# Optimization experiments

Hardware: AMD Instinct MI355X
Metric: run time of the kernel (lower is better)

## Reference

```python
import jax, jax.numpy as jnp
import numpy as np

IN_F, OUT_F, LAT, B = 1024, 1024, 16, 256


def setup_inputs() -> dict:
    key = jax.random.key(0)
    ks = jax.random.split(key, 6)
    # xavier_normal for weight [in, out]
    std_w = float(np.sqrt(2.0 / (IN_F + OUT_F)))
    weight = jax.random.normal(ks[0], (IN_F, OUT_F), dtype=jnp.float32) * std_w
    bias = jnp.full((OUT_F,), 0.01, dtype=jnp.float32)
    # nn.Linear(latent, in): weight [in, latent], bias [in], kaiming-uniform-ish init
    lim = float(1.0 / np.sqrt(LAT))
    lt_w = jax.random.uniform(ks[1], (IN_F, LAT), minval=-lim, maxval=lim, dtype=jnp.float32)
    lt_b = jax.random.uniform(ks[2], (IN_F,), minval=-lim, maxval=lim, dtype=jnp.float32)
    tensor = jax.random.normal(ks[3], (B, IN_F), dtype=jnp.float32)
    z = jax.random.normal(ks[4], (B, LAT), dtype=jnp.float32)
    return {"tensor": tensor, "z": z, "weight": weight, "bias": bias,
            "lt_w": lt_w, "lt_b": lt_b}


def reference(tensor, z, weight, bias, lt_w, lt_b):
    # s = latent_transform(z): [B, in]
    s = z @ lt_w.T + lt_b
    # Demodulation factor: rsqrt(sum_i (s_i * W_io)^2 + eps) = rsqrt((s^2) @ (W^2) + eps)
    # Algebraically identical to forming the per-sample modulated weight, but
    # never materializes the [B, in, out] tensor.
    factor = jax.lax.rsqrt((s * s) @ (weight * weight) + 1e-8)  # [B, out]
    # x @ (W * s[:, :, None]) == (x * s) @ W
    out = ((tensor * s) @ weight) * factor + bias  # [B, out]
    return out
```

## Files before the change

### kernel.cpp

```cpp
#include <hip/hip_runtime.h>
#include <hip/hip_bf16.h>

constexpr int IN_F  = 1024;
constexpr int OUT_F = 1024;
constexpr int LAT   = 16;
constexpr int BATCH = 256;

typedef __attribute__((ext_vector_type(8))) short  bf16x8;
typedef __attribute__((ext_vector_type(4))) float  f32x4;

static __device__ __forceinline__ unsigned short bf16_bits(float v) {
  __hip_bfloat16 h = __float2bfloat16(v);
  return *reinterpret_cast<unsigned short*>(&h);
}
static __device__ __forceinline__ float bf16_f32(unsigned short u) {
  __hip_bfloat16 h;
  *reinterpret_cast<unsigned short*>(&h) = u;
  return __bfloat162float(h);
}

__global__ __launch_bounds__(512) void fused_mod(
    const float* __restrict__ tensor, const float* __restrict__ z,
    const float* __restrict__ lt_w, const float* __restrict__ lt_b,
    const float* __restrict__ W, const float* __restrict__ bias,
    float* __restrict__ out) {
  __shared__ __attribute__((aligned(16))) __hip_bfloat16 s_lds[32 * 1024];
  __shared__ __attribute__((aligned(16))) __hip_bfloat16 wbuf[8][2][32 * 64];

  const int bid = blockIdx.x;
  const int t = threadIdx.x;
  const int n0 = (bid & 31) * 32;
  const int m0 = (bid >> 5) * 32;
  const int lane = t & 63;
  const int wave = t >> 6;
  const int lm = lane & 15;
  const int h = lane >> 4;

  {
    const int koct = h & 1;
    bf16x8 zfrag[2];
#pragma unroll
    for (int bh = 0; bh < 2; ++bh) {
      const float* zp = z + (m0 + bh * 16 + lm) * LAT + koct * 8;
      float4 v0 = *reinterpret_cast<const float4*>(zp);
      float4 v1 = *reinterpret_cast<const float4*>(zp + 4);
      float v[8] = {v0.x, v0.y, v0.z, v0.w, v1.x, v1.y, v1.z, v1.w};
      union { unsigned short u[8]; bf16x8 b; } fz;
#pragma unroll
      for (int j = 0; j < 8; ++j) {
        unsigned short hi = bf16_bits(v[j]);
        fz.u[j] = (h < 2) ? hi : bf16_bits(v[j] - bf16_f32(hi));
      }
      zfrag[bh] = fz.b;
    }
#pragma unroll 4
    for (int itl = 0; itl < 8; ++itl) {
      const int i0 = (wave * 8 + itl) * 16;
      const float* wp = lt_w + (i0 + lm) * LAT + koct * 8;
      float4 v0 = *reinterpret_cast<const float4*>(wp);
      float4 v1 = *reinterpret_cast<const float4*>(wp + 4);
      float v[8] = {v0.x, v0.y, v0.z, v0.w, v1.x, v1.y, v1.z, v1.w};
      union { unsigned short u[8]; bf16x8 b; } f1, f2;
#pragma unroll
      for (int j = 0; j < 8; ++j) {
        unsigned short hi = bf16_bits(v[j]);
        f1.u[j] = hi;
        f2.u[j] = (h < 2) ? bf16_bits(v[j] - bf16_f32(hi)) : 0;
      }
      const float4 bq = *reinterpret_cast<const float4*>(lt_b + i0 + h * 4);
      const int cbase = (i0 >> 3) + (h >> 1);
      const int sub8 = (h & 1) * 8;
#pragma unroll
      for (int bh = 0; bh < 2; ++bh) {
        f32x4 sacc = {0.f, 0.f, 0.f, 0.f};
        sacc = __builtin_amdgcn_mfma_f32_16x16x32_bf16(f1.b, zfrag[bh], sacc, 0, 0, 0);
        sacc = __builtin_amdgcn_mfma_f32_16x16x32_bf16(f2.b, zfrag[bh], sacc, 0, 0, 0);
        const int r = bh * 16 + lm;
        union { unsigned short u[4]; uint2 d; } pk;
        pk.u[0] = bf16_bits(sacc[0] + bq.x);
        pk.u[1] = bf16_bits(sacc[1] + bq.y);
        pk.u[2] = bf16_bits(sacc[2] + bq.z);
        pk.u[3] = bf16_bits(sacc[3] + bq.w);
        const int off = r * 2048 + ((cbase ^ (r & 7)) << 4) + sub8;
        *reinterpret_cast<uint2*>(reinterpret_cast<char*>(s_lds) + off) = pk.d;
      }
    }
  }
  __syncthreads();

  const int sn  = lane & 31;
  const int shb = lane >> 5;

  f32x4 acc1[2][2], acc2[2][2];
#pragma unroll
  for (int mi = 0; mi < 2; ++mi)
#pragma unroll
    for (int ni = 0; ni < 2; ++ni) {
      acc1[mi][ni] = (f32x4){0.f, 0.f, 0.f, 0.f};
      acc2[mi][ni] = (f32x4){0.f, 0.f, 0.f, 0.f};
    }

#pragma unroll
  for (int tt = 0; tt < 2; ++tt) {
    const int k0 = wave * 128 + tt * 64;
    char* wt = reinterpret_cast<char*>(&wbuf[wave][tt & 1][0]);
#pragma unroll
    for (int q = 0; q < 4; ++q) {
      const int koct = shb + 2 * q;
      union { unsigned short u[8]; bf16x8 b; } pw;
#pragma unroll
      for (int j = 0; j < 8; ++j) {
        const float v = W[(k0 + koct * 8 + j) * OUT_F + n0 + sn];
        pw.u[j] = bf16_bits(v);
      }
      const int woff = sn * 128 + ((koct ^ (sn & 7)) << 4);
      *reinterpret_cast<bf16x8*>(wt + woff) = pw.b;
    }
#pragma unroll
    for (int sub = 0; sub < 2; ++sub) {
      const int kk = k0 + sub * 32 + h * 8;
      const int c = kk >> 3;
      union { unsigned short u[8]; bf16x8 b; } fxs0, fss0, fxs1, fss1;
      {
        const int r0 = lm;
        const float* xp0 = tensor + (m0 + r0) * IN_F + kk;
        float4 xa0 = *reinterpret_cast<const float4*>(xp0);
        float4 xb0 = *reinterpret_cast<const float4*>(xp0 + 4);
        bf16x8 s80 = *reinterpret_cast<const bf16x8*>(
            reinterpret_cast<char*>(s_lds) + r0 * 2048 + ((c ^ (r0 & 7)) << 4));
        const float xv0[8] = {xa0.x, xa0.y, xa0.z, xa0.w, xb0.x, xb0.y, xb0.z, xb0.w};
#pragma unroll
        for (int j = 0; j < 8; ++j) {
          const float sf = bf16_f32((unsigned short)s80[j]);
          fxs0.u[j] = bf16_bits(xv0[j] * sf);
          fss0.u[j] = bf16_bits(sf * sf);
        }
        const int r1 = 16 + lm;
        const float* xp1 = tensor + (m0 + r1) * IN_F + kk;
        float4 xa1 = *reinterpret_cast<const float4*>(xp1);
        float4 xb1 = *reinterpret_cast<const float4*>(xp1 + 4);
        bf16x8 s81 = *reinterpret_cast<const bf16x8*>(
            reinterpret_cast<char*>(s_lds) + r1 * 2048 + ((c ^ (r1 & 7)) << 4));
        const float xv1[8] = {xa1.x, xa1.y, xa1.z, xa1.w, xb1.x, xb1.y, xb1.z, xb1.w};
#pragma unroll
        for (int j = 0; j < 8; ++j) {
          const float sf = bf16_f32((unsigned short)s81[j]);
          fxs1.u[j] = bf16_bits(xv1[j] * sf);
          fss1.u[j] = bf16_bits(sf * sf);
        }
      }
#pragma unroll
      for (int ni = 0; ni < 2; ++ni) {
        const int br = ni * 16 + lm;
        const int boff = br * 128 + (((sub * 4 + h) ^ (br & 7)) << 4);
        bf16x8 b1 = *reinterpret_cast<const bf16x8*>(wt + boff);
        union { unsigned short u[8]; bf16x8 b; } b2;
#pragma unroll
        for (int j = 0; j < 8; ++j) {
          const float wv = bf16_f32((unsigned short)b1[j]);
          b2.u[j] = bf16_bits(wv * wv);
        }
        acc1[0][ni] = __builtin_amdgcn_mfma_f32_16x16x32_bf16(fxs0.b, b1,   acc1[0][ni], 0, 0, 0);
        acc2[0][ni] = __builtin_amdgcn_mfma_f32_16x16x32_bf16(fss0.b, b2.b, acc2[0][ni], 0, 0, 0);
        acc1[1][ni] = __builtin_amdgcn_mfma_f32_16x16x32_bf16(fxs1.b, b1,   acc1[1][ni], 0, 0, 0);
        acc2[1][ni] = __builtin_amdgcn_mfma_f32_16x16x32_bf16(fss1.b, b2.b, acc2[1][ni], 0, 0, 0);
      }
    }
  }

  {
    float* cb = reinterpret_cast<float*>(&wbuf[wave][0][0]);
#pragma unroll
    for (int mi = 0; mi < 2; ++mi)
#pragma unroll
      for (int ni = 0; ni < 2; ++ni) {
        const int i1 = mi * 2 + ni;
        *reinterpret_cast<f32x4*>(cb + i1 * 256 + lane * 4) = acc1[mi][ni];
        *reinterpret_cast<f32x4*>(cb + (4 + i1) * 256 + lane * 4) = acc2[mi][ni];
      }
  }
  __syncthreads();

  {
    f32x4 tsum = {0.f, 0.f, 0.f, 0.f};
#pragma unroll
    for (int v = 0; v < 8; ++v) {
      const float* src = reinterpret_cast<const float*>(&wbuf[v][0][0]);
      tsum += *reinterpret_cast<const f32x4*>(src + wave * 256 + lane * 4);
    }
    if (wave >= 4) {
      *reinterpret_cast<f32x4*>(
          reinterpret_cast<float*>(s_lds) + (wave - 4) * 256 + lane * 4) = tsum;
    }
    __syncthreads();
    if (wave < 4) {
      f32x4 t2 = *reinterpret_cast<const f32x4*>(
          reinterpret_cast<const float*>(s_lds) + wave * 256 + lane * 4);
      const int mi = wave >> 1;
      const int ni = wave & 1;
      const int col = n0 + ni * 16 + lm;
      const float bs = bias[col];
#pragma unroll
      for (int q = 0; q < 4; ++q) {
        const int row = m0 + mi * 16 + h * 4 + q;
        out[row * OUT_F + col] = tsum[q] * __frsqrt_rn(t2[q] + 1e-8f) + bs;
      }
    }
  }
}

extern "C" void kernel_launch(void* const* d_in, const int* in_sizes, int n_in,
                              void* d_out, int out_size, void* d_ws, size_t ws_size,
                              hipStream_t stream) {
  const float* tensor = (const float*)d_in[0];
  const float* z      = (const float*)d_in[1];
  const float* W      = (const float*)d_in[2];
  const float* bias   = (const float*)d_in[3];
  const float* lt_w   = (const float*)d_in[4];
  const float* lt_b   = (const float*)d_in[5];
  float* out = (float*)d_out;

  fused_mod<<<256, 512, 0, stream>>>(tensor, z, lt_w, lt_b, W, bias, out);
}
```

Measured before the change: 14.76 us.

## Load W and x fragments directly into registers and prefetch before the s computation

Drops the per-wave LDS staging of W tiles. Each lane now reads its own W column fragments straight into registers in MFMA operand layout. The first k-chunk of W and x is issued before the latent-transform MFMA phase, and the second chunk is prefetched during the first chunk's compute, so global latency is meant to overlap with work. This uses more registers and strided, less coalesced W loads (stride OUT_F per element, 16 lanes contiguous), and the extra register pressure could lower occupancy.

```diff
diff --git a/kernel.cpp b/kernel.cpp
--- a/kernel.cpp
+++ b/kernel.cpp
@@ -25,7 +25,7 @@
     const float* __restrict__ W, const float* __restrict__ bias,
     float* __restrict__ out) {
   __shared__ __attribute__((aligned(16))) __hip_bfloat16 s_lds[32 * 1024];
-  __shared__ __attribute__((aligned(16))) __hip_bfloat16 wbuf[8][2][32 * 64];
+  __shared__ __attribute__((aligned(16))) float cbuf[8 * 2048];
 
   const int bid = blockIdx.x;
   const int t = threadIdx.x;
@@ -35,6 +35,28 @@
   const int wave = t >> 6;
   const int lm = lane & 15;
   const int h = lane >> 4;
+
+  const int kw = wave * 128;
+  float wv[2][2][8];
+  float xr[2][2][8];
+#pragma unroll
+  for (int sub = 0; sub < 2; ++sub) {
+    const int kb = kw + sub * 32 + h * 8;
+#pragma unroll
+    for (int ni = 0; ni < 2; ++ni) {
+      const float* p = W + (size_t)kb * OUT_F + n0 + ni * 16 + lm;
+#pragma unroll
+      for (int j = 0; j < 8; ++j) wv[sub][ni][j] = p[j * OUT_F];
+    }
+#pragma unroll
+    for (int r = 0; r < 2; ++r) {
+      const float* p = tensor + (m0 + r * 16 + lm) * IN_F + kb;
+      float4 a = *reinterpret_cast<const float4*>(p);
+      float4 b = *reinterpret_cast<const float4*>(p + 4);
+      xr[sub][r][0] = a.x; xr[sub][r][1] = a.y; xr[sub][r][2] = a.z; xr[sub][r][3] = a.w;
+      xr[sub][r][4] = b.x; xr[sub][r][5] = b.y; xr[sub][r][6] = b.z; xr[sub][r][7] = b.w;
+    }
+  }
 
   {
     const int koct = h & 1;
@@ -88,9 +110,6 @@
   }
   __syncthreads();
 
-  const int sn  = lane & 31;
-  const int shb = lane >> 5;
-
   f32x4 acc1[2][2], acc2[2][2];
 #pragma unroll
   for (int mi = 0; mi < 2; ++mi)
@@ -102,74 +121,72 @@
 
 #pragma unroll
   for (int tt = 0; tt < 2; ++tt) {
-    const int k0 = wave * 128 + tt * 64;
-    char* wt = reinterpret_cast<char*>(&wbuf[wave][tt & 1][0]);
-#pragma unroll
-    for (int q = 0; q < 4; ++q) {
-      const int koct = shb + 2 * q;
-      union { unsigned short u[8]; bf16x8 b; } pw;
-#pragma unroll
-      for (int j = 0; j < 8; ++j) {
-        const float v = W[(k0 + koct * 8 + j) * OUT_F + n0 + sn];
-        pw.u[j] = bf16_bits(v);
-      }
-      const int woff = sn * 128 + ((koct ^ (sn & 7)) << 4);
-      *reinterpret_cast<bf16x8*>(wt + woff) = pw.b;
-    }
+    const int k0 = kw + tt * 64;
+    bf16x8 s8[2][2];
 #pragma unroll
     for (int sub = 0; sub < 2; ++sub) {
-      const int kk = k0 + sub * 32 + h * 8;
-      const int c = kk >> 3;
-      union { unsigned short u[8]; bf16x8 b; } fxs0, fss0, fxs1, fss1;
-      {
-        const int r0 = lm;
-        const float* xp0 = tensor + (m0 + r0) * IN_F + kk;
-        float4 xa0 = *reinterpret_cast<const float4*>(xp0);
-        float4 xb0 = *reinterpret_cast<const float4*>(xp0 + 4);
-        bf16x8 s80 = *reinterpret_cast<const bf16x8*>(
-            reinterpret_cast<char*>(s_lds) + r0 * 2048 + ((c ^ (r0 & 7)) << 4));
-        const float xv0[8] = {xa0.x, xa0.y, xa0.z, xa0.w, xb0.x, xb0.y, xb0.z, xb0.w};
+      const int c = (k0 + sub * 32 + h * 8) >> 3;
+#pragma unroll
+      for (int r = 0; r < 2; ++r) {
+        const int rr = r * 16 + lm;
+        s8[sub][r] = *reinterpret_cast<const bf16x8*>(
+            reinterpret_cast<char*>(s_lds) + rr * 2048 + ((c ^ (rr & 7)) << 4));
+      }
+    }
+    union { unsigned short u[8]; bf16x8 b; } b1[2][2], b2[2][2], fxs[2][2], fss[2][2];
+#pragma unroll
+    for (int sub = 0; sub < 2; ++sub) {
+#pragma unroll
+      for (int ni = 0; ni < 2; ++ni)
 #pragma unroll
         for (int j = 0; j < 8; ++j) {
-          const float sf = bf16_f32((unsigned short)s80[j]);
-          fxs0.u[j] = bf16_bits(xv0[j] * sf);
-          fss0.u[j] = bf16_bits(sf * sf);
-        }
-        const int r1 = 16 + lm;
-        const float* xp1 = tensor + (m0 + r1) * IN_F + kk;
-        float4 xa1 = *reinterpret_cast<const float4*>(xp1);
-        float4 xb1 = *reinterpret_cast<const float4*>(xp1 + 4);
-        bf16x8 s81 = *reinterpret_cast<const bf16x8*>(
-            reinterpret_cast<char*>(s_lds) + r1 * 2048 + ((c ^ (r1 & 7)) << 4));
-        const float xv1[8] = {xa1.x, xa1.y, xa1.z, xa1.w, xb1.x, xb1.y, xb1.z, xb1.w};
+          const float v = wv[sub][ni][j];
+          b1[sub][ni].u[j] = bf16_bits(v);
+          b2[sub][ni].u[j] = bf16_bits(v * v);
+        }
+#pragma unroll
+      for (int r = 0; r < 2; ++r)
 #pragma unroll
         for (int j = 0; j < 8; ++j) {
-          const float sf = bf16_f32((unsigned short)s81[j]);
-          fxs1.u[j] = bf16_bits(xv1[j] * sf);
-          fss1.u[j] = bf16_bits(sf * sf);
-        }
-      }
+          const float sf = bf16_f32((unsigned short)s8[sub][r][j]);
+          fxs[sub][r].u[j] = bf16_bits(xr[sub][r][j] * sf);
+          fss[sub][r].u[j] = bf16_bits(sf * sf);
+        }
+    }
+    if (tt == 0) {
+      const int kn = kw + 64;
+#pragma unroll
+      for (int sub = 0; sub < 2; ++sub) {
+        const int kb = kn + sub * 32 + h * 8;
+#pragma unroll
+        for (int ni = 0; ni < 2; ++ni) {
+          const float* p = W + (size_t)kb * OUT_F + n0 + ni * 16 + lm;
+#pragma unroll
+          for (int j = 0; j < 8; ++j) wv[sub][ni][j] = p[j * OUT_F];
+        }
+#pragma unroll
+        for (int r = 0; r < 2; ++r) {
+          const float* p = tensor + (m0 + r * 16 + lm) * IN_F + kb;
+          float4 a = *reinterpret_cast<const float4*>(p);
+          float4 b = *reinterpret_cast<const float4*>(p + 4);
+          xr[sub][r][0] = a.x; xr[sub][r][1] = a.y; xr[sub][r][2] = a.z; xr[sub][r][3] = a.w;
+          xr[sub][r][4] = b.x; xr[sub][r][5] = b.y; xr[sub][r][6] = b.z; xr[sub][r][7] = b.w;
+        }
+      }
+    }
+#pragma unroll
+    for (int sub = 0; sub < 2; ++sub)
 #pragma unroll
       for (int ni = 0; ni < 2; ++ni) {
-        const int br = ni * 16 + lm;
-        const int boff = br * 128 + (((sub * 4 + h) ^ (br & 7)) << 4);
-        bf16x8 b1 = *reinterpret_cast<const bf16x8*>(wt + boff);
-        union { unsigned short u[8]; bf16x8 b; } b2;
-#pragma unroll
-        for (int j = 0; j < 8; ++j) {
-          const float wv = bf16_f32((unsigned short)b1[j]);
-          b2.u[j] = bf16_bits(wv * wv);
-        }
-        acc1[0][ni] = __builtin_amdgcn_mfma_f32_16x16x32_bf16(fxs0.b, b1,   acc1[0][ni], 0, 0, 0);
-        acc2[0][ni] = __builtin_amdgcn_mfma_f32_16x16x32_bf16(fss0.b, b2.b, acc2[0][ni], 0, 0, 0);
-        acc1[1][ni] = __builtin_amdgcn_mfma_f32_16x16x32_bf16(fxs1.b, b1,   acc1[1][ni], 0, 0, 0);
-        acc2[1][ni] = __builtin_amdgcn_mfma_f32_16x16x32_bf16(fss1.b, b2.b, acc2[1][ni], 0, 0, 0);
-      }
-    }
+        acc1[0][ni] = __builtin_amdgcn_mfma_f32_16x16x32_bf16(fxs[sub][0].b, b1[sub][ni].b, acc1[0][ni], 0, 0, 0);
+        acc2[0][ni] = __builtin_amdgcn_mfma_f32_16x16x32_bf16(fss[sub][0].b, b2[sub][ni].b, acc2[0][ni], 0, 0, 0);
+        acc1[1][ni] = __builtin_amdgcn_mfma_f32_16x16x32_bf16(fxs[sub][1].b, b1[sub][ni].b, acc1[1][ni], 0, 0, 0);
+        acc2[1][ni] = __builtin_amdgcn_mfma_f32_16x16x32_bf16(fss[sub][1].b, b2[sub][ni].b, acc2[1][ni], 0, 0, 0);
+      }
   }
 
   {
-    float* cb = reinterpret_cast<float*>(&wbuf[wave][0][0]);
+    float* cb = cbuf + wave * 2048;
 #pragma unroll
     for (int mi = 0; mi < 2; ++mi)
 #pragma unroll
@@ -184,10 +201,8 @@
   {
     f32x4 tsum = {0.f, 0.f, 0.f, 0.f};
 #pragma unroll
-    for (int v = 0; v < 8; ++v) {
-      const float* src = reinterpret_cast<const float*>(&wbuf[v][0][0]);
-      tsum += *reinterpret_cast<const f32x4*>(src + wave * 256 + lane * 4);
-    }
+    for (int v = 0; v < 8; ++v)
+      tsum += *reinterpret_cast<const f32x4*>(cbuf + v * 2048 + wave * 256 + lane * 4);
     if (wave >= 4) {
       *reinterpret_cast<f32x4*>(
           reinterpret_cast<float*>(s_lds) + (wave - 4) * 256 + lane * 4) = tsum;
```

Result: slower. 16.04 us (+8.6%).
